# Kernel tuning notes

Hardware: AMD Instinct MI355X
Metric: run time of the kernel (lower is better)

Reference implementation:

```python
import jax, jax.numpy as jnp
import numpy as np


def dwconv3x3(x, w, b):
    # depthwise 3x3, stride 1, padding 1 (SAME); x: [B,C,H,W], w: [C,1,3,3], b: [C]
    y = jax.lax.conv_general_dilated(
        x, w, window_strides=(1, 1), padding='SAME',
        dimension_numbers=('NCHW', 'OIHW', 'NCHW'),
        feature_group_count=x.shape[1])
    return y + b[None, :, None, None]


def setup_inputs() -> dict:
    B, C, K, H, W = 16, 512, 128, 64, 64
    key = jax.random.key(0)
    ks = jax.random.split(key, 8)
    return {
        'x_q': jax.random.normal(ks[0], (B, C, H, W), jnp.float32),
        'x_kv': jax.random.normal(ks[1], (B, K, H, W), jnp.float32),
        'wq': jax.random.normal(ks[2], (C, 1, 3, 3), jnp.float32) * 0.1,
        'bq': jax.random.normal(ks[3], (C,), jnp.float32) * 0.1,
        'wk': jax.random.normal(ks[4], (K, 1, 3, 3), jnp.float32) * 0.1,
        'bk': jax.random.normal(ks[5], (K,), jnp.float32) * 0.1,
        'wv': jax.random.normal(ks[6], (K, 1, 3, 3), jnp.float32) * 0.1,
        'bv': jax.random.normal(ks[7], (K,), jnp.float32) * 0.1,
    }


def reference(x_q, x_kv, wq, bq, wk, bk, wv, bv):
    q = dwconv3x3(x_q, wq, bq)          # [B,C,H,W]
    k = dwconv3x3(x_kv, wk, bk)         # [B,K,H,W]
    v = dwconv3x3(x_kv, wv, bv)         # [B,K,H,W]
    B, C, H, W = q.shape
    Kp = k.shape[1]
    qf = q.reshape(B, C, H * W)         # [B,C,N]
    kf = k.reshape(B, Kp, H * W)        # [B,K,N]
    vf = v.reshape(B, Kp, H * W)        # [B,K,N]
    # attn_weights: [B,C,K], scaled by sqrt(num_prompt)
    aw = jnp.einsum('bcn,bkn->bck', qf, kf) / (Kp ** 0.5)
    aw = jax.nn.softmax(aw, axis=-1)
    n_keep = int(0.1 * C)               # static
    aw_t = jnp.swapaxes(aw, 1, 2)       # [B,K,C]
    _, idx = jax.lax.top_k(aw_t, n_keep)  # idx: [B,K,n_keep]
    bi = jnp.arange(B)[:, None, None]
    ki = jnp.arange(Kp)[None, :, None]
    mask_t = jnp.zeros_like(aw_t).at[bi, ki, idx].set(1.0)
    aw = aw * jnp.swapaxes(mask_t, 1, 2)  # [B,C,K]
    attn_out = jnp.einsum('bck,bkn->bcn', aw, vf).reshape(B, C, H, W)
    return (x_q + attn_out, aw)
```

## Files before the change

### kernel.cpp

```cpp
#include <hip/hip_runtime.h>

#define B_ 16
#define C_ 512
#define K_ 128
#define N_ 4096
#define NKEEP 51
#define NSPLIT 8

__global__ void conv_kv_kernel(const float* __restrict__ xkv,
                               const float* __restrict__ wk, const float* __restrict__ bk,
                               const float* __restrict__ wv, const float* __restrict__ bv,
                               float* __restrict__ kb, float* __restrict__ vb) {
    int idx = blockIdx.x * 256 + threadIdx.x;
    int x = idx & 63;
    int y = (idx >> 6) & 63;
    int k = (idx >> 12) & 127;
    int b = idx >> 19;
    const float* wkp = wk + k * 9;
    const float* wvp = wv + k * 9;
    const float* xp  = xkv + (size_t)(b * K_ + k) * N_;
    float ak = bk[k], av = bv[k];
#pragma unroll
    for (int dy = 0; dy < 3; ++dy) {
        int yy = y + dy - 1;
        if (yy < 0 || yy > 63) continue;
#pragma unroll
        for (int dx = 0; dx < 3; ++dx) {
            int xx = x + dx - 1;
            if (xx < 0 || xx > 63) continue;
            float xv = xp[yy * 64 + xx];
            ak += xv * wkp[dy * 3 + dx];
            av += xv * wvp[dy * 3 + dx];
        }
    }
    kb[idx] = ak;
    vb[idx] = av;
}

__global__ __launch_bounds__(256, 3) void qk3_kernel(const float* __restrict__ xq,
                                                     const float* __restrict__ wq,
                                                     const float* __restrict__ bq,
                                                     const float* __restrict__ kb,
                                                     float* __restrict__ part) {
    __shared__ float qs[64][64];
    __shared__ float ks[64][128];

    int bid = blockIdx.x;
    int blk = (bid & 7) * 128 + (bid >> 3);
    int ct  = blk & 7;
    int ns  = (blk >> 3) & 7;
    int b   = blk >> 6;
    int c0  = ct * 64;
    int r0  = ns * 8;
    int tid = threadIdx.x;

    int c_l = tid >> 2;
    int xs  = (tid & 3) << 4;
    int k_l = tid >> 1;
    int nh  = (tid & 1) << 5;
    int cg4 = (tid & 15) * 4;
    int kg8 = (tid >> 4) * 8;

    const float* wp = wq + (size_t)(c0 + c_l) * 9;
    float w00=wp[0],w01=wp[1],w02=wp[2],w10=wp[3],w11=wp[4],w12=wp[5],w20=wp[6],w21=wp[7],w22=wp[8];
    float bias = bq[c0 + c_l];
    const float* xqp = xq + ((size_t)(b * C_) + c0 + c_l) * N_;
    const float* kbp = kb + ((size_t)(b * K_) + k_l) * N_ + nh;

    float4 kv[8];
    float4 xm[3][4];
    float  xl[3], xr[3];

#define LOADROW(r)                                                             \
    {                                                                          \
        const float4* src = (const float4*)(kbp + (r) * 64);                   \
        _Pragma("unroll")                                                      \
        for (int m = 0; m < 8; ++m) kv[m] = src[m];                            \
        _Pragma("unroll")                                                      \
        for (int dy = 0; dy < 3; ++dy) {                                       \
            int yy = (r) + dy - 1;                                             \
            if (yy < 0 || yy > 63) {                                           \
                _Pragma("unroll")                                              \
                for (int m = 0; m < 4; ++m) xm[dy][m] = make_float4(0,0,0,0);  \
                xl[dy] = 0.f; xr[dy] = 0.f;                                    \
            } else {                                                           \
                const float* row = xqp + yy * 64 + xs;                         \
                const float4* r4 = (const float4*)row;                         \
                _Pragma("unroll")                                              \
                for (int m = 0; m < 4; ++m) xm[dy][m] = r4[m];                 \
                xl[dy] = (xs == 0)  ? 0.f : row[-1];                           \
                xr[dy] = (xs == 48) ? 0.f : row[16];                           \
            }                                                                  \
        }                                                                      \
    }

    float acc[4][8];
#pragma unroll
    for (int i = 0; i < 4; ++i)
#pragma unroll
        for (int j = 0; j < 8; ++j) acc[i][j] = 0.f;

    LOADROW(r0);

    for (int rr = 0; rr < 8; ++rr) {
        __syncthreads();
#pragma unroll
        for (int m = 0; m < 8; ++m) {
            int nn = nh + m * 4;
            ks[nn][k_l]     = kv[m].x; ks[nn + 1][k_l] = kv[m].y;
            ks[nn + 2][k_l] = kv[m].z; ks[nn + 3][k_l] = kv[m].w;
        }
        {
            float a16[16];
#pragma unroll
            for (int i = 0; i < 16; ++i) a16[i] = bias;
#pragma unroll
            for (int dy = 0; dy < 3; ++dy) {
                float wa = (dy == 0) ? w00 : (dy == 1) ? w10 : w20;
                float wb = (dy == 0) ? w01 : (dy == 1) ? w11 : w21;
                float wc = (dy == 0) ? w02 : (dy == 1) ? w12 : w22;
                float xrow[18];
                xrow[0] = xl[dy];
#pragma unroll
                for (int m = 0; m < 4; ++m) {
                    xrow[1 + 4*m]     = xm[dy][m].x;
                    xrow[1 + 4*m + 1] = xm[dy][m].y;
                    xrow[1 + 4*m + 2] = xm[dy][m].z;
                    xrow[1 + 4*m + 3] = xm[dy][m].w;
                }
                xrow[17] = xr[dy];
#pragma unroll
                for (int i = 0; i < 16; ++i)
                    a16[i] += xrow[i] * wa + xrow[i + 1] * wb + xrow[i + 2] * wc;
            }
#pragma unroll
            for (int i = 0; i < 16; ++i) qs[xs + i][c_l] = a16[i];
        }
        __syncthreads();
        if (rr < 7) LOADROW(r0 + rr + 1);
#pragma unroll 4
        for (int nn = 0; nn < 64; ++nn) {
            float4 q4  = *(const float4*)&qs[nn][cg4];
            float4 k4a = *(const float4*)&ks[nn][kg8];
            float4 k4b = *(const float4*)&ks[nn][kg8 + 4];
            float qa[4] = {q4.x, q4.y, q4.z, q4.w};
            float kk[8] = {k4a.x, k4a.y, k4a.z, k4a.w, k4b.x, k4b.y, k4b.z, k4b.w};
#pragma unroll
            for (int i = 0; i < 4; ++i)
#pragma unroll
                for (int j = 0; j < 8; ++j) acc[i][j] += qa[i] * kk[j];
        }
    }
#undef LOADROW

    float* dst = part + (((size_t)ns * B_ + b) * C_ + c0 + cg4) * K_ + kg8;
#pragma unroll
    for (int i = 0; i < 4; ++i) {
        *(float4*)(dst + (size_t)i * K_)     = make_float4(acc[i][0], acc[i][1], acc[i][2], acc[i][3]);
        *(float4*)(dst + (size_t)i * K_ + 4) = make_float4(acc[i][4], acc[i][5], acc[i][6], acc[i][7]);
    }
}

__global__ void softmax_kernel(const float* __restrict__ part, float* __restrict__ aw) {
    int tid  = threadIdx.x;
    int wave = tid >> 6;
    int lane = tid & 63;
    int row  = blockIdx.x * 4 + wave;
    float v0 = 0.f, v1 = 0.f;
#pragma unroll
    for (int ns = 0; ns < NSPLIT; ++ns) {
        const float* p = part + ((size_t)ns * B_ * C_ + row) * K_;
        v0 += p[lane];
        v1 += p[lane + 64];
    }
    const float scale = 0.08838834764831845f;
    v0 *= scale; v1 *= scale;
    float m = fmaxf(v0, v1);
#pragma unroll
    for (int s = 32; s >= 1; s >>= 1) m = fmaxf(m, __shfl_xor(m, s, 64));
    float e0 = __expf(v0 - m), e1 = __expf(v1 - m);
    float s = e0 + e1;
#pragma unroll
    for (int t = 32; t >= 1; t >>= 1) s += __shfl_xor(s, t, 64);
    float inv = 1.0f / s;
    float* q = aw + (size_t)row * K_;
    q[lane] = e0 * inv;
    q[lane + 64] = e1 * inv;
}

__global__ void topk_mask_kernel(float* __restrict__ aw) {
    int tid  = threadIdx.x;
    int wave = tid >> 6, lane = tid & 63;
    int col  = blockIdx.x * 4 + wave;
    int b = col >> 7, k = col & 127;
    float* base = aw + (size_t)(b * C_) * K_ + k;
    unsigned u[8];
#pragma unroll
    for (int j = 0; j < 8; ++j)
        u[j] = __float_as_uint(base[(size_t)(j * 64 + lane) * K_]);
    unsigned T = 0;
#pragma unroll
    for (int bit = 31; bit >= 0; --bit) {
        unsigned cand = T | (1u << bit);
        int cnt = 0;
#pragma unroll
        for (int j = 0; j < 8; ++j) cnt += (u[j] >= cand) ? 1 : 0;
#pragma unroll
        for (int s = 32; s >= 1; s >>= 1) cnt += __shfl_xor(cnt, s, 64);
        if (cnt >= NKEEP) T = cand;
    }
#pragma unroll
    for (int j = 0; j < 8; ++j)
        if (u[j] < T) base[(size_t)(j * 64 + lane) * K_] = 0.0f;
}

__global__ __launch_bounds__(256) void av_kernel(const float* __restrict__ aw,
                                                 const float* __restrict__ vb,
                                                 const float* __restrict__ xq,
                                                 float* __restrict__ out) {
    __shared__ float vs[16][260];
    __shared__ float aws[16][36];
    int blk  = blockIdx.x;
    int b    = blk >> 8;
    int rest = blk & 255;
    int c0 = (rest >> 4) * 32;
    int n0 = (rest & 15) * 256;
    int tid = threadIdx.x;
    int cg = tid >> 5;
    int ng = tid & 31;
    int k_l = tid >> 4;
    int nn0 = (tid & 15) * 16;
    int i0  = tid * 2;
    int cc0 = i0 >> 4,       kk0 = i0 & 15;
    int cc1 = (i0 + 1) >> 4, kk1 = (i0 + 1) & 15;

    float4 vv[4];
    float  a0, a1;

#define LOADAV(kc)                                                              \
    {                                                                           \
        const float4* src = (const float4*)(vb + (size_t)(b * K_ + (kc) + k_l) * N_ + n0 + nn0); \
        _Pragma("unroll")                                                       \
        for (int m = 0; m < 4; ++m) vv[m] = src[m];                             \
        a0 = aw[(size_t)(b * C_ + c0 + cc0) * K_ + (kc) + kk0];                 \
        a1 = aw[(size_t)(b * C_ + c0 + cc1) * K_ + (kc) + kk1];                 \
    }

    float acc[4][8];
#pragma unroll
    for (int i = 0; i < 4; ++i)
#pragma unroll
        for (int j = 0; j < 8; ++j) acc[i][j] = 0.f;

    LOADAV(0);

    for (int kc = 0; kc < K_; kc += 16) {
        __syncthreads();
        {
            float4* dst = (float4*)&vs[k_l][nn0];
#pragma unroll
            for (int m = 0; m < 4; ++m) dst[m] = vv[m];
            aws[kk0][cc0] = a0;
            aws[kk1][cc1] = a1;
        }
        __syncthreads();
        if (kc + 16 < K_) LOADAV(kc + 16);
#pragma unroll
        for (int kk = 0; kk < 16; ++kk) {
            float4 a4  = *(const float4*)&aws[kk][cg * 4];
            float4 v4a = *(const float4*)&vs[kk][ng * 8];
            float4 v4b = *(const float4*)&vs[kk][ng * 8 + 4];
            float aa[4] = {a4.x, a4.y, a4.z, a4.w};
            float av[8] = {v4a.x, v4a.y, v4a.z, v4a.w, v4b.x, v4b.y, v4b.z, v4b.w};
#pragma unroll
            for (int i = 0; i < 4; ++i)
#pragma unroll
                for (int j = 0; j < 8; ++j) acc[i][j] += aa[i] * av[j];
        }
    }
#undef LOADAV

#pragma unroll
    for (int i = 0; i < 4; ++i) {
        int c = c0 + cg * 4 + i;
        size_t base = (size_t)(b * C_ + c) * N_ + n0 + ng * 8;
        const float4* xp4 = (const float4*)(xq + base);
        float4* op4 = (float4*)(out + base);
        float4 x0 = xp4[0], x1 = xp4[1];
        float4 o0, o1;
        o0.x = x0.x + acc[i][0]; o0.y = x0.y + acc[i][1];
        o0.z = x0.z + acc[i][2]; o0.w = x0.w + acc[i][3];
        o1.x = x1.x + acc[i][4]; o1.y = x1.y + acc[i][5];
        o1.z = x1.z + acc[i][6]; o1.w = x1.w + acc[i][7];
        op4[0] = o0; op4[1] = o1;
    }
}

extern "C" void kernel_launch(void* const* d_in, const int* in_sizes, int n_in,
                              void* d_out, int out_size, void* d_ws, size_t ws_size,
                              hipStream_t stream) {
    const float* xq  = (const float*)d_in[0];
    const float* xkv = (const float*)d_in[1];
    const float* wq  = (const float*)d_in[2];
    const float* bq  = (const float*)d_in[3];
    const float* wk  = (const float*)d_in[4];
    const float* bk  = (const float*)d_in[5];
    const float* wv  = (const float*)d_in[6];
    const float* bv  = (const float*)d_in[7];

    float* out0 = (float*)d_out;
    float* aw   = out0 + (size_t)B_ * C_ * N_;

    float* kb = (float*)d_ws;
    float* vb = kb + (size_t)B_ * K_ * N_;
    float* part = out0;

    conv_kv_kernel<<<(B_ * K_ * N_) / 256, 256, 0, stream>>>(xkv, wk, bk, wv, bv, kb, vb);
    qk3_kernel<<<B_ * 64, 256, 0, stream>>>(xq, wq, bq, kb, part);
    softmax_kernel<<<(B_ * C_) / 4, 256, 0, stream>>>(part, aw);
    topk_mask_kernel<<<(B_ * K_) / 4, 256, 0, stream>>>(aw);
    av_kernel<<<B_ * 256, 256, 0, stream>>>(aw, vb, xq, out0);
}
```

Before: 634.2 us.

## Vectorize kv depthwise conv, software-pipeline q conv in qk, tune av occupancy

Result: slower. 717.9 us (+13.2%).

```diff
diff --git a/kernel.cpp b/kernel.cpp
--- a/kernel.cpp
+++ b/kernel.cpp
@@ -7,37 +7,55 @@
 #define NKEEP 51
 #define NSPLIT 8
 
-__global__ void conv_kv_kernel(const float* __restrict__ xkv,
+__global__ __launch_bounds__(256) void conv_kv_kernel(const float* __restrict__ xkv,
                                const float* __restrict__ wk, const float* __restrict__ bk,
                                const float* __restrict__ wv, const float* __restrict__ bv,
                                float* __restrict__ kb, float* __restrict__ vb) {
     int idx = blockIdx.x * 256 + threadIdx.x;
-    int x = idx & 63;
-    int y = (idx >> 6) & 63;
-    int k = (idx >> 12) & 127;
-    int b = idx >> 19;
+    int xs = (idx & 3) << 4;
+    int y  = (idx >> 2) & 63;
+    int k  = (idx >> 8) & 127;
+    int b  = idx >> 15;
     const float* wkp = wk + k * 9;
     const float* wvp = wv + k * 9;
     const float* xp  = xkv + (size_t)(b * K_ + k) * N_;
-    float ak = bk[k], av = bv[k];
+    float ak[16], av[16];
+    float bk0 = bk[k], bv0 = bv[k];
+#pragma unroll
+    for (int i = 0; i < 16; ++i) { ak[i] = bk0; av[i] = bv0; }
 #pragma unroll
     for (int dy = 0; dy < 3; ++dy) {
         int yy = y + dy - 1;
         if (yy < 0 || yy > 63) continue;
-#pragma unroll
-        for (int dx = 0; dx < 3; ++dx) {
-            int xx = x + dx - 1;
-            if (xx < 0 || xx > 63) continue;
-            float xv = xp[yy * 64 + xx];
-            ak += xv * wkp[dy * 3 + dx];
-            av += xv * wvp[dy * 3 + dx];
-        }
-    }
-    kb[idx] = ak;
-    vb[idx] = av;
-}
-
-__global__ __launch_bounds__(256, 3) void qk3_kernel(const float* __restrict__ xq,
+        const float* row = xp + yy * 64 + xs;
+        const float4* r4 = (const float4*)row;
+        float4 m0 = r4[0], m1 = r4[1], m2 = r4[2], m3 = r4[3];
+        float xrow[18];
+        xrow[0] = (xs == 0) ? 0.f : row[-1];
+        xrow[1] = m0.x;  xrow[2] = m0.y;  xrow[3] = m0.z;  xrow[4] = m0.w;
+        xrow[5] = m1.x;  xrow[6] = m1.y;  xrow[7] = m1.z;  xrow[8] = m1.w;
+        xrow[9] = m2.x;  xrow[10] = m2.y; xrow[11] = m2.z; xrow[12] = m2.w;
+        xrow[13] = m3.x; xrow[14] = m3.y; xrow[15] = m3.z; xrow[16] = m3.w;
+        xrow[17] = (xs == 48) ? 0.f : row[16];
+        float ka = wkp[dy * 3], kb_ = wkp[dy * 3 + 1], kc_ = wkp[dy * 3 + 2];
+        float va = wvp[dy * 3], vb_ = wvp[dy * 3 + 1], vc_ = wvp[dy * 3 + 2];
+#pragma unroll
+        for (int i = 0; i < 16; ++i) {
+            ak[i] += xrow[i] * ka + xrow[i + 1] * kb_ + xrow[i + 2] * kc_;
+            av[i] += xrow[i] * va + xrow[i + 1] * vb_ + xrow[i + 2] * vc_;
+        }
+    }
+    size_t o = (size_t)(b * K_ + k) * N_ + y * 64 + xs;
+    float4* kd = (float4*)(kb + o);
+    float4* vd = (float4*)(vb + o);
+#pragma unroll
+    for (int m = 0; m < 4; ++m) {
+        kd[m] = make_float4(ak[4*m], ak[4*m+1], ak[4*m+2], ak[4*m+3]);
+        vd[m] = make_float4(av[4*m], av[4*m+1], av[4*m+2], av[4*m+3]);
+    }
+}
+
+__global__ __launch_bounds__(256, 3) void qk4_kernel(const float* __restrict__ xq,
                                                      const float* __restrict__ wq,
                                                      const float* __restrict__ bq,
                                                      const float* __restrict__ kb,
@@ -70,37 +88,67 @@
     float4 kv[8];
     float4 xm[3][4];
     float  xl[3], xr[3];
-
-#define LOADROW(r)                                                             \
+    float  a16[16];
+
+#define LOADK(r)                                                               \
     {                                                                          \
-        const float4* src = (const float4*)(kbp + (r) * 64);                   \
+        const float4* src_ = (const float4*)(kbp + (r) * 64);                  \
         _Pragma("unroll")                                                      \
-        for (int m = 0; m < 8; ++m) kv[m] = src[m];                            \
+        for (int m = 0; m < 8; ++m) kv[m] = src_[m];                           \
+    }
+
+#define XLOAD(t)                                                               \
+    {                                                                          \
         _Pragma("unroll")                                                      \
         for (int dy = 0; dy < 3; ++dy) {                                       \
-            int yy = (r) + dy - 1;                                             \
+            int yy = (t) + dy - 1;                                             \
             if (yy < 0 || yy > 63) {                                           \
                 _Pragma("unroll")                                              \
                 for (int m = 0; m < 4; ++m) xm[dy][m] = make_float4(0,0,0,0);  \
                 xl[dy] = 0.f; xr[dy] = 0.f;                                    \
             } else {                                                           \
-                const float* row = xqp + yy * 64 + xs;                         \
-                const float4* r4 = (const float4*)row;                         \
+                const float* row_ = xqp + yy * 64 + xs;                        \
+                const float4* r4_ = (const float4*)row_;                       \
                 _Pragma("unroll")                                              \
-                for (int m = 0; m < 4; ++m) xm[dy][m] = r4[m];                 \
-                xl[dy] = (xs == 0)  ? 0.f : row[-1];                           \
-                xr[dy] = (xs == 48) ? 0.f : row[16];                           \
+                for (int m = 0; m < 4; ++m) xm[dy][m] = r4_[m];                \
+                xl[dy] = (xs == 0)  ? 0.f : row_[-1];                          \
+                xr[dy] = (xs == 48) ? 0.f : row_[16];                          \
             }                                                                  \
         }                                                                      \
     }
 
+#define CONVMATH()                                                             \
+    {                                                                          \
+        _Pragma("unroll")                                                      \
+        for (int i = 0; i < 16; ++i) a16[i] = bias;                            \
+        _Pragma("unroll")                                                      \
+        for (int dy = 0; dy < 3; ++dy) {                                       \
+            float wa = (dy == 0) ? w00 : (dy == 1) ? w10 : w20;                \
+            float wb = (dy == 0) ? w01 : (dy == 1) ? w11 : w21;                \
+            float wc = (dy == 0) ? w02 : (dy == 1) ? w12 : w22;                \
+            float xrow[18];                                                    \
+            xrow[0] = xl[dy];                                                  \
+            _Pragma("unroll")                                                  \
+            for (int m = 0; m < 4; ++m) {                                      \
+                xrow[1 + 4*m] = xm[dy][m].x; xrow[2 + 4*m] = xm[dy][m].y;      \
+                xrow[3 + 4*m] = xm[dy][m].z; xrow[4 + 4*m] = xm[dy][m].w;      \
+            }                                                                  \
+            xrow[17] = xr[dy];                                                 \
+            _Pragma("unroll")                                                  \
+            for (int i = 0; i < 16; ++i)                                       \
+                a16[i] += xrow[i] * wa + xrow[i + 1] * wb + xrow[i + 2] * wc;  \
+        }                                                                      \
+    }
+
     float acc[4][8];
 #pragma unroll
     for (int i = 0; i < 4; ++i)
 #pragma unroll
         for (int j = 0; j < 8; ++j) acc[i][j] = 0.f;
 
-    LOADROW(r0);
+    LOADK(r0);
+    XLOAD(r0);
+    CONVMATH();
 
     for (int rr = 0; rr < 8; ++rr) {
         __syncthreads();
@@ -110,34 +158,10 @@
             ks[nn][k_l]     = kv[m].x; ks[nn + 1][k_l] = kv[m].y;
             ks[nn + 2][k_l] = kv[m].z; ks[nn + 3][k_l] = kv[m].w;
         }
-        {
-            float a16[16];
-#pragma unroll
-            for (int i = 0; i < 16; ++i) a16[i] = bias;
-#pragma unroll
-            for (int dy = 0; dy < 3; ++dy) {
-                float wa = (dy == 0) ? w00 : (dy == 1) ? w10 : w20;
-                float wb = (dy == 0) ? w01 : (dy == 1) ? w11 : w21;
-                float wc = (dy == 0) ? w02 : (dy == 1) ? w12 : w22;
-                float xrow[18];
-                xrow[0] = xl[dy];
-#pragma unroll
-                for (int m = 0; m < 4; ++m) {
-                    xrow[1 + 4*m]     = xm[dy][m].x;
-                    xrow[1 + 4*m + 1] = xm[dy][m].y;
-                    xrow[1 + 4*m + 2] = xm[dy][m].z;
-                    xrow[1 + 4*m + 3] = xm[dy][m].w;
-                }
-                xrow[17] = xr[dy];
-#pragma unroll
-                for (int i = 0; i < 16; ++i)
-                    a16[i] += xrow[i] * wa + xrow[i + 1] * wb + xrow[i + 2] * wc;
-            }
-#pragma unroll
-            for (int i = 0; i < 16; ++i) qs[xs + i][c_l] = a16[i];
-        }
+#pragma unroll
+        for (int i = 0; i < 16; ++i) qs[xs + i][c_l] = a16[i];
         __syncthreads();
-        if (rr < 7) LOADROW(r0 + rr + 1);
+        if (rr < 7) { LOADK(r0 + rr + 1); XLOAD(r0 + rr + 1); }
 #pragma unroll 4
         for (int nn = 0; nn < 64; ++nn) {
             float4 q4  = *(const float4*)&qs[nn][cg4];
@@ -150,8 +174,11 @@
 #pragma unroll
                 for (int j = 0; j < 8; ++j) acc[i][j] += qa[i] * kk[j];
         }
-    }
-#undef LOADROW
+        if (rr < 7) CONVMATH();
+    }
+#undef LOADK
+#undef XLOAD
+#undef CONVMATH
 
     float* dst = part + (((size_t)ns * B_ + b) * C_ + c0 + cg4) * K_ + kg8;
 #pragma unroll
@@ -214,7 +241,7 @@
         if (u[j] < T) base[(size_t)(j * 64 + lane) * K_] = 0.0f;
 }
 
-__global__ __launch_bounds__(256) void av_kernel(const float* __restrict__ aw,
+__global__ __launch_bounds__(256, 3) void av_kernel(const float* __restrict__ aw,
                                                  const float* __restrict__ vb,
                                                  const float* __restrict__ xq,
                                                  float* __restrict__ out) {
@@ -315,8 +342,8 @@
     float* vb = kb + (size_t)B_ * K_ * N_;
     float* part = out0;
 
-    conv_kv_kernel<<<(B_ * K_ * N_) / 256, 256, 0, stream>>>(xkv, wk, bk, wv, bv, kb, vb);
-    qk3_kernel<<<B_ * 64, 256, 0, stream>>>(xq, wq, bq, kb, part);
+    conv_kv_kernel<<<(B_ * K_ * 64 * 4) / 256, 256, 0, stream>>>(xkv, wk, bk, wv, bv, kb, vb);
+    qk4_kernel<<<B_ * 64, 256, 0, stream>>>(xq, wq, bq, kb, part);
     softmax_kernel<<<(B_ * C_) / 4, 256, 0, stream>>>(part, aw);
     topk_mask_kernel<<<(B_ * K_) / 4, 256, 0, stream>>>(aw);
     av_kernel<<<B_ * 256, 256, 0, stream>>>(aw, vb, xq, out0);
```
